# Performance work log

Measured on AMD Instinct MI355X. Metric: run time of the kernel, lower is better.

The kernel has to match this reference:

```python
import jax, jax.numpy as jnp
import numpy as np

VOCAB = 32000
B, S = 1, 2048
D = 1024          # emb_dim == qkv_dim
H = 16            # num_heads
HD = D // H       # head_dim = 64
M = 4096          # mlp_dim
L = 4             # num_layers
WIN = 512         # sliding_window_size
HALF = WIN // 2   # attend to |i-j| <= HALF
N_GLOBAL = 64
EPS = 1e-6


def sinusoidal_pos_emb(max_len, d, max_scale=10000.0):
    pos = np.arange(max_len)[:, None].astype(np.float32)
    div = np.exp(np.arange(0, d, 2).astype(np.float32) * (-np.log(max_scale) / d))
    pe = np.zeros((max_len, d), dtype=np.float32)
    pe[:, 0::2] = np.sin(pos * div)
    pe[:, 1::2] = np.cos(pos * div)
    return jnp.asarray(pe)


def layer_norm(x, scale, bias):
    mu = jnp.mean(x, axis=-1, keepdims=True)
    var = jnp.mean(jnp.square(x - mu), axis=-1, keepdims=True)
    return (x - mu) * jax.lax.rsqrt(var + EPS) * scale + bias


def setup_inputs() -> dict:
    key = jax.random.key(0)
    ks = jax.random.split(key, 16)
    inputs = jax.random.randint(ks[0], (B, S), 0, VOCAB, dtype=jnp.int32)
    gm = jnp.zeros((B, S), dtype=bool).at[:, :N_GLOBAL].set(True)
    std = 0.02
    return {
        'inputs': inputs,
        'global_mask': gm,
        'embed': jax.random.normal(ks[1], (VOCAB, D), jnp.float32),
        'wq': jax.random.normal(ks[2], (L, D, H, HD), jnp.float32) * std,
        'wk': jax.random.normal(ks[3], (L, D, H, HD), jnp.float32) * std,
        'wv': jax.random.normal(ks[4], (L, D, H, HD), jnp.float32) * std,
        'wo': jax.random.normal(ks[5], (L, H, HD, D), jnp.float32) * std,
        'ln1_s': jnp.ones((L, D), jnp.float32),
        'ln1_b': jnp.zeros((L, D), jnp.float32),
        'ln2_s': jnp.ones((L, D), jnp.float32),
        'ln2_b': jnp.zeros((L, D), jnp.float32),
        'w1': jax.random.normal(ks[6], (L, D, M), jnp.float32) * std,
        'b1': jnp.zeros((L, M), jnp.float32),
        'w2': jax.random.normal(ks[7], (L, M, D), jnp.float32) * std,
        'b2': jnp.zeros((L, D), jnp.float32),
        'lnf_s': jnp.ones((D,), jnp.float32),
        'lnf_b': jnp.zeros((D,), jnp.float32),
    }


def _attention_mask(global_mask):
    idx = jnp.arange(S)
    band = jnp.abs(idx[:, None] - idx[None, :]) <= HALF           # [S, S]
    allowed = band[None, :, :] | global_mask[:, :, None] | global_mask[:, None, :]
    return allowed[:, None, :, :]                                  # [B, 1, S, S]


def forward(inputs, global_mask, embed, wq, wk, wv, wo, ln1_s, ln1_b,
            ln2_s, ln2_b, w1, b1, w2, b2, lnf_s, lnf_b):
    x = embed[inputs]                                # [B, S, D]
    x = x + sinusoidal_pos_emb(S, D)[None]
    mask = _attention_mask(global_mask)              # [B, 1, S, S]
    neg = jnp.asarray(-1e9, x.dtype)
    scale = 1.0 / jnp.sqrt(jnp.asarray(HD, x.dtype))
    for l in range(L):
        h = layer_norm(x, ln1_s[l], ln1_b[l])
        q = jnp.einsum('bsd,dhk->bshk', h, wq[l]) * scale
        k = jnp.einsum('bsd,dhk->bshk', h, wk[l])
        v = jnp.einsum('bsd,dhk->bshk', h, wv[l])
        scores = jnp.einsum('bqhk,bshk->bhqs', q, k)         # [B, H, S, S]
        scores = jnp.where(mask, scores, neg)
        probs = jax.nn.softmax(scores, axis=-1)
        ctx = jnp.einsum('bhqs,bshk->bqhk', probs, v)
        attn_out = jnp.einsum('bqhk,hkd->bqd', ctx, wo[l])
        x = x + attn_out
        y = layer_norm(x, ln2_s[l], ln2_b[l])
        y = jax.nn.relu(jnp.einsum('bsd,dm->bsm', y, w1[l]) + b1[l])
        y = jnp.einsum('bsm,md->bsd', y, w2[l]) + b2[l]
        x = x + y
    return layer_norm(x, lnf_s, lnf_b)


def reference(inputs, global_mask, embed, wq, wk, wv, wo, ln1_s, ln1_b,
              ln2_s, ln2_b, w1, b1, w2, b2, lnf_s, lnf_b):
    return forward(inputs, global_mask, embed, wq, wk, wv, wo, ln1_s, ln1_b,
                   ln2_s, ln2_b, w1, b1, w2, b2, lnf_s, lnf_b)
```

## Files before the change

### kernel.cpp

```cpp
#include <hip/hip_runtime.h>
#include <hip/hip_bf16.h>

typedef __attribute__((ext_vector_type(8))) short bf16x8;
typedef __attribute__((ext_vector_type(4))) float f32x4;

__device__ __forceinline__ ushort f2bf(float f) {
    union { float f; uint u; } v; v.f = f;
    uint r = v.u + 0x7FFF + ((v.u >> 16) & 1);
    return (ushort)(r >> 16);
}

__device__ __forceinline__ void ld16(const void* g, void* l) {
    __builtin_amdgcn_global_load_lds(
        (const __attribute__((address_space(1))) void*)g,
        (__attribute__((address_space(3))) void*)l, 16, 0, 0);
}

__global__ __launch_bounds__(256) void conv_w_kernel(
    const float* __restrict__ src, ushort* __restrict__ dst,
    int K, int N, float scale)
{
    __shared__ ushort Ts[64][65];
    const int tid = threadIdx.x;
    const int n0 = blockIdx.x * 64;
    const int k0 = blockIdx.y * 64;
    const int c4 = tid & 15;
    const int r0 = tid >> 4;
    #pragma unroll
    for (int it = 0; it < 4; it++) {
        int r = r0 + it * 16;
        float4 v = *(const float4*)(src + (size_t)(k0 + r) * N + n0 + c4 * 4);
        Ts[c4 * 4 + 0][r] = f2bf(v.x * scale);
        Ts[c4 * 4 + 1][r] = f2bf(v.y * scale);
        Ts[c4 * 4 + 2][r] = f2bf(v.z * scale);
        Ts[c4 * 4 + 3][r] = f2bf(v.w * scale);
    }
    __syncthreads();
    #pragma unroll
    for (int it = 0; it < 4; it++) {
        int nr = r0 + it * 16;
        uint lo = (uint)Ts[nr][c4 * 4 + 0] | ((uint)Ts[nr][c4 * 4 + 1] << 16);
        uint hi = (uint)Ts[nr][c4 * 4 + 2] | ((uint)Ts[nr][c4 * 4 + 3] << 16);
        uint2 w = make_uint2(lo, hi);
        *(uint2*)(dst + (size_t)(n0 + nr) * K + k0 + c4 * 4) = w;
    }
}

template<int TN>
__global__ __launch_bounds__(256) void gemm_t(
    const ushort* __restrict__ A, const ushort* __restrict__ Bt,
    const float* __restrict__ bias, const float* resid,
    float* outF, ushort* outB, int M, int N, int K, int ldk, int relu,
    float* __restrict__ outP)
{
    __shared__ ushort As[4][128 * 32];
    __shared__ ushort Bs[4][TN * 32];
    const int tid  = threadIdx.x;
    const int lane = tid & 63;
    const int wave = tid >> 6;
    const int quad = lane >> 4;
    const int lr   = lane & 15;
    const int wm   = wave >> 1;
    const int wn   = wave & 1;
    constexpr int NT = (TN == 128) ? 4 : 2;
    const int bm0 = blockIdx.x * 128;
    const int bn0 = blockIdx.y * TN;
    const int kz  = blockIdx.z * K;

    f32x4 acc[4][NT];
    #pragma unroll
    for (int i = 0; i < 4; i++)
        #pragma unroll
        for (int j = 0; j < NT; j++)
            acc[i][j] = (f32x4){0.f, 0.f, 0.f, 0.f};

    const ushort* gA = A  + (size_t)(bm0 + (tid >> 2)) * ldk + kz + (tid & 3) * 8;
    const ushort* gB = Bt + (size_t)(bn0 + (tid >> 2)) * ldk + kz + (tid & 3) * 8;

    auto stage = [&](int b, int k) {
        ushort* la = &As[b][wave * 512];
        ushort* lb = &Bs[b][wave * 512];
        ld16(gA + k, la);
        ld16(gA + k + (size_t)64 * ldk, la + 2048);
        ld16(gB + k, lb);
        if constexpr (TN == 128) ld16(gB + k + (size_t)64 * ldk, lb + 2048);
    };
    auto step = [&](int b, int t3) {
        bf16x8 aF[4], bF[NT];
        const ushort* as = As[b];
        const ushort* bs = Bs[b];
        #pragma unroll
        for (int mt = 0; mt < 4; mt++)
            aF[mt] = *(const bf16x8*)&as[(wm * 64 + mt * 16 + lr) * 32 + quad * 8];
        #pragma unroll
        for (int nt = 0; nt < NT; nt++)
            bF[nt] = *(const bf16x8*)&bs[(wn * (TN / 2) + nt * 16 + lr) * 32 + quad * 8];
        if (t3 >= 0) stage(t3 & 3, t3 * 32);
        #pragma unroll
        for (int mt = 0; mt < 4; mt++)
            #pragma unroll
            for (int nt = 0; nt < NT; nt++)
                acc[mt][nt] = __builtin_amdgcn_mfma_f32_16x16x32_bf16(
                    aF[mt], bF[nt], acc[mt][nt], 0, 0, 0);
    };

    const int ntk = K >> 5;
    stage(0, 0); stage(1, 32); stage(2, 64);
    for (int t = 0; t < ntk - 2; ++t) {
        if constexpr (TN == 128) asm volatile("s_waitcnt vmcnt(8)" ::: "memory");
        else                     asm volatile("s_waitcnt vmcnt(6)" ::: "memory");
        __builtin_amdgcn_s_barrier();
        step(t & 3, (t + 3 < ntk) ? (t + 3) : -1);
    }
    if constexpr (TN == 128) asm volatile("s_waitcnt vmcnt(4)" ::: "memory");
    else                     asm volatile("s_waitcnt vmcnt(3)" ::: "memory");
    __builtin_amdgcn_s_barrier();
    step((ntk - 2) & 3, -1);
    asm volatile("s_waitcnt vmcnt(0)" ::: "memory");
    __builtin_amdgcn_s_barrier();
    step((ntk - 1) & 3, -1);

    if (outP) {
        float* dst = outP + (size_t)blockIdx.z * M * N;
        #pragma unroll
        for (int mt = 0; mt < 4; mt++) {
            #pragma unroll
            for (int nt = 0; nt < NT; nt++) {
                int col  = bn0 + wn * (TN / 2) + nt * 16 + lr;
                int rowb = bm0 + wm * 64 + mt * 16 + quad * 4;
                #pragma unroll
                for (int r = 0; r < 4; r++)
                    dst[(size_t)(rowb + r) * N + col] = acc[mt][nt][r];
            }
        }
        return;
    }

    #pragma unroll
    for (int mt = 0; mt < 4; mt++) {
        #pragma unroll
        for (int nt = 0; nt < NT; nt++) {
            int col  = bn0 + wn * (TN / 2) + nt * 16 + lr;
            int rowb = bm0 + wm * 64 + mt * 16 + quad * 4;
            #pragma unroll
            for (int r = 0; r < 4; r++) {
                int row = rowb + r;
                float v = acc[mt][nt][r];
                if (bias)  v += bias[col];
                if (resid) v += resid[(size_t)row * N + col];
                if (relu)  v = fmaxf(v, 0.f);
                if (outF)  outF[(size_t)row * N + col] = v;
                else       outB[(size_t)row * N + col] = f2bf(v);
            }
        }
    }
}

__global__ __launch_bounds__(256) void reduceK_kernel(
    const float* __restrict__ part, int nsplit,
    const float* __restrict__ bias, const float* __restrict__ resid,
    float* __restrict__ outF, int N)
{
    const int row = blockIdx.x;
    const int col = threadIdx.x * 4;
    const size_t off = (size_t)row * N + col;
    const size_t stride = (size_t)2048 * N;
    float4 a = *(const float4*)(part + off);
    for (int s = 1; s < nsplit; s++) {
        float4 b = *(const float4*)(part + (size_t)s * stride + off);
        a.x += b.x; a.y += b.y; a.z += b.z; a.w += b.w;
    }
    if (bias) {
        a.x += bias[col]; a.y += bias[col + 1];
        a.z += bias[col + 2]; a.w += bias[col + 3];
    }
    if (resid) {
        float4 r = *(const float4*)(resid + off);
        a.x += r.x; a.y += r.y; a.z += r.z; a.w += r.w;
    }
    *(float4*)(outF + off) = a;
}

#define LDA 72

__global__ __launch_bounds__(256) void attn_mfma_kernel(
    const ushort* __restrict__ qkv, ushort* __restrict__ Cm,
    float* __restrict__ po, float* __restrict__ pm, float* __restrict__ pl)
{
    const int bx   = blockIdx.x;
    const int h    = blockIdx.y;
    const int sp   = (bx >= 31);
    const int qt   = sp ? 0 : bx + 1;
    const int s    = sp ? bx - 31 : 0;
    const int tid  = threadIdx.x;
    const int lane = tid & 63;
    const int wave = tid >> 6;
    const int quad = lane >> 4;
    const int lr   = lane & 15;
    const int q0   = qt * 64;

    __shared__ ushort Qs[64 * LDA];
    __shared__ ushort Ks[64 * LDA];
    __shared__ ushort Vt[64 * LDA];
    __shared__ ushort Ps[64 * LDA];

    {
        int ql = tid >> 2, d0 = (tid & 3) * 16;
        const ushort* qp = qkv + (size_t)(q0 + ql) * 3072 + h * 64 + d0;
        *(uint4*)&Qs[ql * LDA + d0]     = *(const uint4*)qp;
        *(uint4*)&Qs[ql * LDA + d0 + 8] = *(const uint4*)(qp + 8);
    }
    __syncthreads();

    bf16x8 aQ[2];
    #pragma unroll
    for (int kc = 0; kc < 2; kc++)
        aQ[kc] = *(const bf16x8*)&Qs[(wave * 16 + lr) * LDA + kc * 32 + quad * 8];

    f32x4 o[4];
    #pragma unroll
    for (int nt = 0; nt < 4; nt++) o[nt] = (f32x4){0.f, 0.f, 0.f, 0.f};
    float m_[4], l_[4];
    #pragma unroll
    for (int r = 0; r < 4; r++) { m_[r] = -1e30f; l_[r] = 0.f; }

    int kt0 = 0, kt1 = 0, ntiles;
    if (sp) {
        ntiles = 8;
    } else {
        kt0 = qt - 4; if (kt0 < 1)  kt0 = 1;
        kt1 = qt + 4; if (kt1 > 31) kt1 = 31;
        ntiles = 1 + (kt1 - kt0 + 1);
    }

    for (int idx = 0; idx < ntiles; idx++) {
        int kt, maskF;
        if (sp) { kt = s * 8 + idx; maskF = 0; }
        else if (idx == 0) { kt = 0; maskF = 0; }
        else { kt = kt0 + idx - 1; maskF = (kt == qt - 4) || (kt == qt + 4); }

        __syncthreads();

        {
            int kl = tid >> 2, d0 = (tid & 3) * 16;
            const ushort* kp = qkv + (size_t)(kt * 64 + kl) * 3072 + 1024 + h * 64 + d0;
            *(uint4*)&Ks[kl * LDA + d0]     = *(const uint4*)kp;
            *(uint4*)&Ks[kl * LDA + d0 + 8] = *(const uint4*)(kp + 8);
        }
        {
            int kp2 = tid & 31, dc = tid >> 5, d0v = dc * 8;
            const ushort* vp = qkv + (size_t)(kt * 64 + 2 * kp2) * 3072 + 2048 + h * 64 + d0v;
            ushort va[8], vb[8];
            *(uint4*)va = *(const uint4*)vp;
            *(uint4*)vb = *(const uint4*)(vp + 3072);
            #pragma unroll
            for (int i = 0; i < 8; i++) {
                uint w = (uint)va[i] | ((uint)vb[i] << 16);
                *(uint*)&Vt[(d0v + i) * LDA + 2 * kp2] = w;
            }
        }
        __syncthreads();

        f32x4 sAcc[4];
        #pragma unroll
        for (int nt = 0; nt < 4; nt++) sAcc[nt] = (f32x4){0.f, 0.f, 0.f, 0.f};
        #pragma unroll
        for (int kc = 0; kc < 2; kc++) {
            #pragma unroll
            for (int nt = 0; nt < 4; nt++) {
                bf16x8 bK = *(const bf16x8*)&Ks[(nt * 16 + lr) * LDA + kc * 32 + quad * 8];
                sAcc[nt] = __builtin_amdgcn_mfma_f32_16x16x32_bf16(aQ[kc], bK, sAcc[nt], 0, 0, 0);
            }
        }

        if (maskF) {
            #pragma unroll
            for (int nt = 0; nt < 4; nt++) {
                int j = kt * 64 + lr + nt * 16;
                #pragma unroll
                for (int r = 0; r < 4; r++) {
                    int q = q0 + wave * 16 + quad * 4 + r;
                    int d = q - j; if (d < 0) d = -d;
                    if (d > 256) sAcc[nt][r] = -1e30f;
                }
            }
        }

        float rmax[4];
        #pragma unroll
        for (int r = 0; r < 4; r++) {
            float v = fmaxf(fmaxf(sAcc[0][r], sAcc[1][r]), fmaxf(sAcc[2][r], sAcc[3][r]));
            v = fmaxf(v, __shfl_xor(v, 1));
            v = fmaxf(v, __shfl_xor(v, 2));
            v = fmaxf(v, __shfl_xor(v, 4));
            v = fmaxf(v, __shfl_xor(v, 8));
            rmax[r] = v;
        }
        float alpha[4];
        #pragma unroll
        for (int r = 0; r < 4; r++) {
            float mn = fmaxf(m_[r], rmax[r]);
            alpha[r] = __expf(m_[r] - mn);
            m_[r] = mn;
        }
        float psum[4] = {0.f, 0.f, 0.f, 0.f};
        #pragma unroll
        for (int nt = 0; nt < 4; nt++)
            #pragma unroll
            for (int r = 0; r < 4; r++) {
                float p = __expf(sAcc[nt][r] - m_[r]);
                sAcc[nt][r] = p;
                psum[r] += p;
            }
        #pragma unroll
        for (int r = 0; r < 4; r++) {
            float v = psum[r];
            v += __shfl_xor(v, 1);
            v += __shfl_xor(v, 2);
            v += __shfl_xor(v, 4);
            v += __shfl_xor(v, 8);
            l_[r] = l_[r] * alpha[r] + v;
        }
        #pragma unroll
        for (int nt = 0; nt < 4; nt++)
            #pragma unroll
            for (int r = 0; r < 4; r++)
                o[nt][r] *= alpha[r];

        #pragma unroll
        for (int nt = 0; nt < 4; nt++)
            #pragma unroll
            for (int r = 0; r < 4; r++)
                Ps[(wave * 16 + quad * 4 + r) * LDA + lr + nt * 16] = f2bf(sAcc[nt][r]);
        __syncthreads();

        #pragma unroll
        for (int kc = 0; kc < 2; kc++) {
            bf16x8 aP = *(const bf16x8*)&Ps[(wave * 16 + lr) * LDA + kc * 32 + quad * 8];
            #pragma unroll
            for (int nt = 0; nt < 4; nt++) {
                bf16x8 bV = *(const bf16x8*)&Vt[(nt * 16 + lr) * LDA + kc * 32 + quad * 8];
                o[nt] = __builtin_amdgcn_mfma_f32_16x16x32_bf16(aP, bV, o[nt], 0, 0, 0);
            }
        }
    }

    if (!sp) {
        #pragma unroll
        for (int nt = 0; nt < 4; nt++) {
            int dim = lr + nt * 16;
            #pragma unroll
            for (int r = 0; r < 4; r++) {
                int row = q0 + wave * 16 + quad * 4 + r;
                Cm[(size_t)row * 1024 + h * 64 + dim] = f2bf(o[nt][r] / l_[r]);
            }
        }
    } else {
        const int base = (h * 4 + s) * 64;
        #pragma unroll
        for (int nt = 0; nt < 4; nt++) {
            int dim = lr + nt * 16;
            #pragma unroll
            for (int r = 0; r < 4; r++) {
                int row = wave * 16 + quad * 4 + r;
                po[(size_t)(base + row) * 64 + dim] = o[nt][r];
            }
        }
        if (lr == 0) {
            #pragma unroll
            for (int r = 0; r < 4; r++) {
                int row = wave * 16 + quad * 4 + r;
                pm[base + row] = m_[r];
                pl[base + row] = l_[r];
            }
        }
    }
}

__global__ __launch_bounds__(256) void attn_combine_kernel(
    const float* __restrict__ po, const float* __restrict__ pm,
    const float* __restrict__ pl, ushort* __restrict__ Cm)
{
    const int h   = blockIdx.x;
    const int tid = threadIdx.x;
    const int row = tid >> 2;
    const int d0  = (tid & 3) * 16;
    float m[4], l[4];
    #pragma unroll
    for (int s = 0; s < 4; s++) {
        m[s] = pm[(h * 4 + s) * 64 + row];
        l[s] = pl[(h * 4 + s) * 64 + row];
    }
    float M = fmaxf(fmaxf(m[0], m[1]), fmaxf(m[2], m[3]));
    float w[4], L = 0.f;
    #pragma unroll
    for (int s = 0; s < 4; s++) { w[s] = __expf(m[s] - M); L += l[s] * w[s]; }
    float inv = 1.0f / L;
    #pragma unroll
    for (int dd = 0; dd < 16; dd += 4) {
        float a0 = 0.f, a1 = 0.f, a2 = 0.f, a3 = 0.f;
        #pragma unroll
        for (int s = 0; s < 4; s++) {
            float4 v = *(const float4*)&po[(size_t)((h * 4 + s) * 64 + row) * 64 + d0 + dd];
            a0 += v.x * w[s]; a1 += v.y * w[s]; a2 += v.z * w[s]; a3 += v.w * w[s];
        }
        ushort* out = &Cm[(size_t)row * 1024 + h * 64 + d0 + dd];
        out[0] = f2bf(a0 * inv); out[1] = f2bf(a1 * inv);
        out[2] = f2bf(a2 * inv); out[3] = f2bf(a3 * inv);
    }
}

__global__ __launch_bounds__(256) void ln_kernel(
    const float* __restrict__ X, const float* __restrict__ gs,
    const float* __restrict__ gb, ushort* outB, float* outF)
{
    const int row = blockIdx.x;
    const int tid = threadIdx.x;
    const int lane = tid & 63;
    const int wave = tid >> 6;
    __shared__ float red[8];

    const float* x = X + (size_t)row * 1024;
    float4 v = *(const float4*)(x + tid * 4);
    float s1 = v.x + v.y + v.z + v.w;
    float s2 = v.x * v.x + v.y * v.y + v.z * v.z + v.w * v.w;
    #pragma unroll
    for (int off = 32; off > 0; off >>= 1) {
        s1 += __shfl_down(s1, off);
        s2 += __shfl_down(s2, off);
    }
    if (lane == 0) { red[wave] = s1; red[4 + wave] = s2; }
    __syncthreads();
    float S1 = red[0] + red[1] + red[2] + red[3];
    float S2 = red[4] + red[5] + red[6] + red[7];
    float mu  = S1 * (1.0f / 1024.0f);
    float var = S2 * (1.0f / 1024.0f) - mu * mu;
    float inv = rsqrtf(var + 1e-6f);
    const float* vp = (const float*)&v;
    #pragma unroll
    for (int i = 0; i < 4; i++) {
        int d = tid * 4 + i;
        float val = (vp[i] - mu) * inv * gs[d] + gb[d];
        if (outF) outF[(size_t)row * 1024 + d] = val;
        else      outB[(size_t)row * 1024 + d] = f2bf(val);
    }
}

__global__ __launch_bounds__(256) void embed_kernel(
    const int* __restrict__ ids, const float* __restrict__ emb,
    float* __restrict__ x)
{
    const int row = blockIdx.x;
    const int tid = threadIdx.x;
    const int id  = ids[row];
    const float c = 0.0089944731f;
    #pragma unroll
    for (int i = 0; i < 4; i++) {
        int d  = tid * 4 + i;
        int de = d & ~1;
        float dv  = __expf(-c * (float)de);
        float ang = (float)row * dv;
        float pe  = (d & 1) ? cosf(ang) : sinf(ang);
        x[(size_t)row * 1024 + d] = emb[(size_t)id * 1024 + d] + pe;
    }
}

extern "C" void kernel_launch(void* const* d_in, const int* in_sizes, int n_in,
                              void* d_out, int out_size, void* d_ws, size_t ws_size,
                              hipStream_t stream)
{
    const int*   ids   = (const int*)d_in[0];
    const float* embed = (const float*)d_in[2];
    const float* wq    = (const float*)d_in[3];
    const float* wk    = (const float*)d_in[4];
    const float* wv    = (const float*)d_in[5];
    const float* wo    = (const float*)d_in[6];
    const float* ln1s  = (const float*)d_in[7];
    const float* ln1b  = (const float*)d_in[8];
    const float* ln2s  = (const float*)d_in[9];
    const float* ln2b  = (const float*)d_in[10];
    const float* w1    = (const float*)d_in[11];
    const float* b1    = (const float*)d_in[12];
    const float* w2    = (const float*)d_in[13];
    const float* b2    = (const float*)d_in[14];
    const float* lnfs  = (const float*)d_in[15];
    const float* lnfb  = (const float*)d_in[16];

    char* ws = (char*)d_ws;
    float*  x   = (float*)ws;
    ushort* h   = (ushort*)(ws + (size_t)(8  << 20));
    ushort* qkv = (ushort*)(ws + (size_t)(12 << 20));
    ushort* ctx = (ushort*)(ws + (size_t)(24 << 20));
    ushort* wb  = (ushort*)(ws + (size_t)(28 << 20));
    float*  po  = (float*)(ws + (size_t)(8  << 20));
    float*  pm  = (float*)(ws + (size_t)(9  << 20));
    float*  pl  = (float*)(ws + (size_t)(9  << 20) + (1 << 16));
    float*  pK  = (float*)(ws + (size_t)(40 << 20));
    ushort* y1  = qkv;

    const dim3 blk(256);

    embed_kernel<<<2048, blk, 0, stream>>>(ids, embed, x);

    for (int l = 0; l < 4; l++) {
        const float* wq_l = wq + (size_t)l * 1024 * 1024;
        const float* wk_l = wk + (size_t)l * 1024 * 1024;
        const float* wv_l = wv + (size_t)l * 1024 * 1024;
        const float* wo_l = wo + (size_t)l * 1024 * 1024;
        const float* w1_l = w1 + (size_t)l * 1024 * 4096;
        const float* w2_l = w2 + (size_t)l * 4096 * 1024;

        ln_kernel<<<2048, blk, 0, stream>>>(x, ln1s + l * 1024, ln1b + l * 1024, h, nullptr);

        conv_w_kernel<<<dim3(16, 16), blk, 0, stream>>>(wq_l, wb,                1024, 1024, 0.125f);
        conv_w_kernel<<<dim3(16, 16), blk, 0, stream>>>(wk_l, wb + 1024 * 1024,  1024, 1024, 1.0f);
        conv_w_kernel<<<dim3(16, 16), blk, 0, stream>>>(wv_l, wb + 2048 * 1024,  1024, 1024, 1.0f);
        gemm_t<128><<<dim3(16, 24), blk, 0, stream>>>(h, wb, nullptr, nullptr,
                                                      nullptr, qkv, 2048, 3072, 1024, 1024, 0, nullptr);

        attn_mfma_kernel<<<dim3(35, 16), blk, 0, stream>>>(qkv, ctx, po, pm, pl);
        attn_combine_kernel<<<dim3(16), blk, 0, stream>>>(po, pm, pl, ctx);

        conv_w_kernel<<<dim3(16, 16), blk, 0, stream>>>(wo_l, wb, 1024, 1024, 1.0f);
        gemm_t<64><<<dim3(16, 16, 2), blk, 0, stream>>>(ctx, wb, nullptr, nullptr,
                                                        nullptr, nullptr, 2048, 1024, 512, 1024, 0, pK);
        reduceK_kernel<<<2048, blk, 0, stream>>>(pK, 2, nullptr, x, x, 1024);

        ln_kernel<<<2048, blk, 0, stream>>>(x, ln2s + l * 1024, ln2b + l * 1024, h, nullptr);

        conv_w_kernel<<<dim3(64, 16), blk, 0, stream>>>(w1_l, wb, 1024, 4096, 1.0f);
        gemm_t<128><<<dim3(16, 32), blk, 0, stream>>>(h, wb, b1 + (size_t)l * 4096, nullptr,
                                                      nullptr, y1, 2048, 4096, 1024, 1024, 1, nullptr);

        conv_w_kernel<<<dim3(16, 64), blk, 0, stream>>>(w2_l, wb, 4096, 1024, 1.0f);
        gemm_t<64><<<dim3(16, 16, 4), blk, 0, stream>>>(y1, wb, nullptr, nullptr,
                                                        nullptr, nullptr, 2048, 1024, 1024, 4096, 0, pK);
        reduceK_kernel<<<2048, blk, 0, stream>>>(pK, 4, b2 + (size_t)l * 1024, x, x, 1024);
    }

    ln_kernel<<<2048, blk, 0, stream>>>(x, lnfs, lnfb, nullptr, (float*)d_out);
}
```

Baseline: 1.071 ms.

## Convert all layer weights in one launch and fuse split-K reduce with layernorm

All per-layer weight conversions (fp32 to bf16, transposed) are merged into a single upfront kernel that writes every layer's weights into one large workspace region, replacing 24 small launches. The split-K reduction kernels now also compute the following layernorm (ln2, the next layer's ln1, or the final norm), which removes the separate ln launches and an extra pass over x. Variance uses E[x^2]-mu^2 in fp32, which is slightly less numerically robust, and the workspace grows to hold about 96MB of bf16 weights.

```diff
diff --git a/kernel.cpp b/kernel.cpp
--- a/kernel.cpp
+++ b/kernel.cpp
@@ -16,14 +16,42 @@
         (__attribute__((address_space(3))) void*)l, 16, 0, 0);
 }
 
-__global__ __launch_bounds__(256) void conv_w_kernel(
-    const float* __restrict__ src, ushort* __restrict__ dst,
-    int K, int N, float scale)
+__global__ __launch_bounds__(256) void conv_all_kernel(
+    const float* __restrict__ wq, const float* __restrict__ wk,
+    const float* __restrict__ wv, const float* __restrict__ wo,
+    const float* __restrict__ w1, const float* __restrict__ w2,
+    ushort* __restrict__ wbAll)
 {
     __shared__ ushort Ts[64][65];
-    const int tid = threadIdx.x;
-    const int n0 = blockIdx.x * 64;
-    const int k0 = blockIdx.y * 64;
+    const int tid   = threadIdx.x;
+    const int idx   = blockIdx.x;
+    const int l     = idx / 3072;
+    const int local = idx - l * 3072;
+    ushort* wbL = wbAll + (size_t)l * 12 * 1024 * 1024;
+
+    const float* src; ushort* dst; int K, N, nb, kb; float scale = 1.0f;
+    if (local < 1024) {
+        int job = local >> 8;
+        int j   = local & 255;
+        nb = j & 15; kb = j >> 4;
+        K = 1024; N = 1024;
+        if (job == 0)      { src = wq + (size_t)l * 1048576; dst = wbL;                 scale = 0.125f; }
+        else if (job == 1) { src = wk + (size_t)l * 1048576; dst = wbL + 1024 * 1024; }
+        else if (job == 2) { src = wv + (size_t)l * 1048576; dst = wbL + 2048 * 1024; }
+        else               { src = wo + (size_t)l * 1048576; dst = wbL + 3072 * 1024; }
+    } else if (local < 2048) {
+        int j = local - 1024;
+        nb = j & 63; kb = j >> 6;
+        K = 1024; N = 4096;
+        src = w1 + (size_t)l * 4194304; dst = wbL + 4 * 1024 * 1024;
+    } else {
+        int j = local - 2048;
+        nb = j & 15; kb = j >> 4;
+        K = 4096; N = 1024;
+        src = w2 + (size_t)l * 4194304; dst = wbL + 8 * 1024 * 1024;
+    }
+    const int n0 = nb * 64;
+    const int k0 = kb * 64;
     const int c4 = tid & 15;
     const int r0 = tid >> 4;
     #pragma unroll
@@ -156,29 +184,59 @@
     }
 }
 
-__global__ __launch_bounds__(256) void reduceK_kernel(
+__global__ __launch_bounds__(256) void reduce_ln_kernel(
     const float* __restrict__ part, int nsplit,
     const float* __restrict__ bias, const float* __restrict__ resid,
-    float* __restrict__ outF, int N)
-{
-    const int row = blockIdx.x;
-    const int col = threadIdx.x * 4;
-    const size_t off = (size_t)row * N + col;
-    const size_t stride = (size_t)2048 * N;
+    float* __restrict__ xout,
+    const float* __restrict__ gs, const float* __restrict__ gb,
+    ushort* outB, float* outF)
+{
+    const int row  = blockIdx.x;
+    const int tid  = threadIdx.x;
+    const int lane = tid & 63;
+    const int wave = tid >> 6;
+    __shared__ float red[8];
+
+    const int col = tid * 4;
+    const size_t off = (size_t)row * 1024 + col;
+    const size_t stride = (size_t)2048 * 1024;
     float4 a = *(const float4*)(part + off);
     for (int s = 1; s < nsplit; s++) {
         float4 b = *(const float4*)(part + (size_t)s * stride + off);
         a.x += b.x; a.y += b.y; a.z += b.z; a.w += b.w;
     }
     if (bias) {
-        a.x += bias[col]; a.y += bias[col + 1];
+        a.x += bias[col];     a.y += bias[col + 1];
         a.z += bias[col + 2]; a.w += bias[col + 3];
     }
-    if (resid) {
+    {
         float4 r = *(const float4*)(resid + off);
         a.x += r.x; a.y += r.y; a.z += r.z; a.w += r.w;
     }
-    *(float4*)(outF + off) = a;
+    *(float4*)(xout + off) = a;
+
+    float s1 = a.x + a.y + a.z + a.w;
+    float s2 = a.x * a.x + a.y * a.y + a.z * a.z + a.w * a.w;
+    #pragma unroll
+    for (int o = 32; o > 0; o >>= 1) {
+        s1 += __shfl_down(s1, o);
+        s2 += __shfl_down(s2, o);
+    }
+    if (lane == 0) { red[wave] = s1; red[4 + wave] = s2; }
+    __syncthreads();
+    float S1 = red[0] + red[1] + red[2] + red[3];
+    float S2 = red[4] + red[5] + red[6] + red[7];
+    float mu  = S1 * (1.0f / 1024.0f);
+    float var = S2 * (1.0f / 1024.0f) - mu * mu;
+    float inv = rsqrtf(var + 1e-6f);
+    const float* ap = (const float*)&a;
+    #pragma unroll
+    for (int i = 0; i < 4; i++) {
+        int d = col + i;
+        float val = (ap[i] - mu) * inv * gs[d] + gb[d];
+        if (outF) outF[(size_t)row * 1024 + d] = val;
+        else      outB[(size_t)row * 1024 + d] = f2bf(val);
+    }
 }
 
 #define LDA 72
@@ -487,56 +545,50 @@
     const float* lnfb  = (const float*)d_in[16];
 
     char* ws = (char*)d_ws;
-    float*  x   = (float*)ws;
-    ushort* h   = (ushort*)(ws + (size_t)(8  << 20));
-    ushort* qkv = (ushort*)(ws + (size_t)(12 << 20));
-    ushort* ctx = (ushort*)(ws + (size_t)(24 << 20));
-    ushort* wb  = (ushort*)(ws + (size_t)(28 << 20));
-    float*  po  = (float*)(ws + (size_t)(8  << 20));
-    float*  pm  = (float*)(ws + (size_t)(9  << 20));
-    float*  pl  = (float*)(ws + (size_t)(9  << 20) + (1 << 16));
-    float*  pK  = (float*)(ws + (size_t)(40 << 20));
-    ushort* y1  = qkv;
+    float*  x    = (float*)ws;
+    ushort* h    = (ushort*)(ws + (size_t)(8  << 20));
+    ushort* qkv  = (ushort*)(ws + (size_t)(12 << 20));
+    ushort* ctx  = (ushort*)(ws + (size_t)(24 << 20));
+    float*  po   = (float*)(ws + (size_t)(8  << 20));
+    float*  pm   = (float*)(ws + (size_t)(9  << 20));
+    float*  pl   = (float*)(ws + (size_t)(9  << 20) + (1 << 16));
+    float*  pK   = (float*)(ws + (size_t)(40 << 20));
+    ushort* wbAll= (ushort*)(ws + (size_t)(80 << 20));
+    ushort* y1   = qkv;
 
     const dim3 blk(256);
 
+    conv_all_kernel<<<12288, blk, 0, stream>>>(wq, wk, wv, wo, w1, w2, wbAll);
+
     embed_kernel<<<2048, blk, 0, stream>>>(ids, embed, x);
+    ln_kernel<<<2048, blk, 0, stream>>>(x, ln1s, ln1b, h, nullptr);
 
     for (int l = 0; l < 4; l++) {
-        const float* wq_l = wq + (size_t)l * 1024 * 1024;
-        const float* wk_l = wk + (size_t)l * 1024 * 1024;
-        const float* wv_l = wv + (size_t)l * 1024 * 1024;
-        const float* wo_l = wo + (size_t)l * 1024 * 1024;
-        const float* w1_l = w1 + (size_t)l * 1024 * 4096;
-        const float* w2_l = w2 + (size_t)l * 4096 * 1024;
-
-        ln_kernel<<<2048, blk, 0, stream>>>(x, ln1s + l * 1024, ln1b + l * 1024, h, nullptr);
-
-        conv_w_kernel<<<dim3(16, 16), blk, 0, stream>>>(wq_l, wb,                1024, 1024, 0.125f);
-        conv_w_kernel<<<dim3(16, 16), blk, 0, stream>>>(wk_l, wb + 1024 * 1024,  1024, 1024, 1.0f);
-        conv_w_kernel<<<dim3(16, 16), blk, 0, stream>>>(wv_l, wb + 2048 * 1024,  1024, 1024, 1.0f);
-        gemm_t<128><<<dim3(16, 24), blk, 0, stream>>>(h, wb, nullptr, nullptr,
+        ushort* wbL = wbAll + (size_t)l * 12 * 1024 * 1024;
+
+        gemm_t<128><<<dim3(16, 24), blk, 0, stream>>>(h, wbL, nullptr, nullptr,
                                                       nullptr, qkv, 2048, 3072, 1024, 1024, 0, nullptr);
 
         attn_mfma_kernel<<<dim3(35, 16), blk, 0, stream>>>(qkv, ctx, po, pm, pl);
         attn_combine_kernel<<<dim3(16), blk, 0, stream>>>(po, pm, pl, ctx);
 
-        conv_w_kernel<<<dim3(16, 16), blk, 0, stream>>>(wo_l, wb, 1024, 1024, 1.0f);
-        gemm_t<64><<<dim3(16, 16, 2), blk, 0, stream>>>(ctx, wb, nullptr, nullptr,
+        gemm_t<64><<<dim3(16, 16, 2), blk, 0, stream>>>(ctx, wbL + 3072 * 1024, nullptr, nullptr,
                                                         nullptr, nullptr, 2048, 1024, 512, 1024, 0, pK);
-        reduceK_kernel<<<2048, blk, 0, stream>>>(pK, 2, nullptr, x, x, 1024);
-
-        ln_kernel<<<2048, blk, 0, stream>>>(x, ln2s + l * 1024, ln2b + l * 1024, h, nullptr);
-
-        conv_w_kernel<<<dim3(64, 16), blk, 0, stream>>>(w1_l, wb, 1024, 4096, 1.0f);
-        gemm_t<128><<<dim3(16, 32), blk, 0, stream>>>(h, wb, b1 + (size_t)l * 4096, nullptr,
+        reduce_ln_kernel<<<2048, blk, 0, stream>>>(pK, 2, nullptr, x, x,
+                                                   ln2s + l * 1024, ln2b + l * 1024, h, nullptr);
+
+        gemm_t<128><<<dim3(16, 32), blk, 0, stream>>>(h, wbL + 4 * 1024 * 1024,
+                                                      b1 + (size_t)l * 4096, nullptr,
                                                       nullptr, y1, 2048, 4096, 1024, 1024, 1, nullptr);
 
-        conv_w_kernel<<<dim3(16, 64), blk, 0, stream>>>(w2_l, wb, 4096, 1024, 1.0f);
-        gemm_t<64><<<dim3(16, 16, 4), blk, 0, stream>>>(y1, wb, nullptr, nullptr,
+        gemm_t<64><<<dim3(16, 16, 4), blk, 0, stream>>>(y1, wbL + 8 * 1024 * 1024, nullptr, nullptr,
                                                         nullptr, nullptr, 2048, 1024, 1024, 4096, 0, pK);
-        reduceK_kernel<<<2048, blk, 0, stream>>>(pK, 4, b2 + (size_t)l * 1024, x, x, 1024);
-    }
-
-    ln_kernel<<<2048, blk, 0, stream>>>(x, lnfs, lnfb, nullptr, (float*)d_out);
-}
+        if (l < 3)
+            reduce_ln_kernel<<<2048, blk, 0, stream>>>(pK, 4, b2 + (size_t)l * 1024, x, x,
+                                                       ln1s + (l + 1) * 1024, ln1b + (l + 1) * 1024,
+                                                       h, nullptr);
+        else
+            reduce_ln_kernel<<<2048, blk, 0, stream>>>(pK, 4, b2 + (size_t)l * 1024, x, x,
+                                                       lnfs, lnfb, nullptr, (float*)d_out);
+    }
+}
```

New measurement: 1.045 ms. -2.4%, faster.
